# Optimization experiments

Hardware: AMD Instinct MI355X
Metric: run time of the kernel (lower is better)

## Reference

```python
import jax, jax.numpy as jnp
import numpy as np
from jax import lax

B, T, IN, H = 128, 1024, 256, 256


def setup_inputs() -> dict:
    key = jax.random.key(0)
    k1, k2, k3, k4 = jax.random.split(key, 4)
    return {
        "fullx": jax.random.normal(k1, (B, T, IN), dtype=jnp.float32),
        "h": jnp.zeros((B, H), dtype=jnp.float32),
        "c": jnp.zeros((B, H), dtype=jnp.float32),
        "wx": jax.random.normal(k2, (IN, 4 * H), dtype=jnp.float32) / (IN ** 0.5),
        "wh": jax.random.normal(k3, (H, 4 * H), dtype=jnp.float32) / (H ** 0.5),
        "b": jax.random.uniform(k4, (1, 4 * H), dtype=jnp.float32),
    }


def reference(fullx, h, c, wx, wh, b):
    hnum = h.shape[1]

    def step(carry, x_t):
        h, c = carry
        t = x_t @ wx + h @ wh + b  # [B, 4H]
        gate = jax.nn.sigmoid(t[:, : 3 * hnum])
        f = gate[:, :hnum]
        i = gate[:, hnum : 2 * hnum]
        o = gate[:, 2 * hnum : 3 * hnum]
        g = jnp.tanh(t[:, 3 * hnum : 4 * hnum])
        c_new = c * f + g * i
        h_new = jnp.tanh(c_new) * o
        return (h_new, c_new), h_new

    xs = jnp.swapaxes(fullx, 0, 1)  # [T, B, IN]
    (h_f, c_f), hs = lax.scan(step, (h, c), xs)
    fullh = jnp.swapaxes(hs, 0, 1)  # [B, T, H]
    return (fullh, h_f, c_f)
```

## Files before the change

kernel.cpp:

```cpp
#include <hip/hip_runtime.h>
#include <hip/hip_fp16.h>
#include <stdint.h>

#define Tdim 1024
#define INdim 256
#define Hdim 256
#define COLS 1024
#define NSLICE 8
#define NGRP 8
#define GB 16
#define UPB 32
#define CPB 128
#define NTHREADS 512
#define FLAG_STRIDE ((Tdim + 1) * NSLICE)
#define FLAG_BYTES (NGRP * FLAG_STRIDE * 4)
#define HBUF_OFF 266240

typedef _Float16 half8 __attribute__((ext_vector_type(8)));
typedef float f32x4 __attribute__((ext_vector_type(4)));

__device__ __forceinline__ uint16_t f2h(float f) {
    __half h = __float2half(f);
    return *reinterpret_cast<uint16_t*>(&h);
}
__device__ __forceinline__ uint32_t pk2(float lo, float hi) {
    return (uint32_t)f2h(lo) | ((uint32_t)f2h(hi) << 16);
}
__device__ __forceinline__ float sigm(float v) {
    return __builtin_amdgcn_rcpf(1.f + __expf(-v));
}
__device__ __forceinline__ float tanhfast(float v) {
    float e = __expf(2.f * v);
    return 1.f - 2.f * __builtin_amdgcn_rcpf(e + 1.f);
}
__device__ __forceinline__ size_t hb_idx(int par, int grp, int m, int u) {
    return ((((size_t)par * NGRP + grp) * GB + m) << 8) | (size_t)u;
}

__global__ __launch_bounds__(NTHREADS, 1) void lstm_main(
    const float* __restrict__ x, const float* __restrict__ h0,
    const float* __restrict__ c0, const float* __restrict__ wx,
    const float* __restrict__ wh, const float* __restrict__ bias,
    float* __restrict__ out, uint32_t* flags, uint16_t* hbuf)
{
    const int tid   = threadIdx.x;
    const int grp   = blockIdx.x & 7;
    const int slice = blockIdx.x >> 3;
    const int lane  = tid & 63;
    const int wave  = tid >> 6;
    const int cw    = lane & 15;
    const int lhi   = lane >> 4;
    const int cl    = wave * 16 + cw;
    const int g     = cl & 3;
    const int ul    = cl >> 2;
    const int u     = slice * UPB + ul;
    const int gcol  = g * Hdim + u;

    __shared__ __align__(16) uint16_t Wl[CPB * 512];
    __shared__ __align__(16) uint16_t X[2][GB][32][8];
    __shared__ __align__(16) uint16_t Hs[GB][32][8];
    __shared__ __align__(16) uint16_t Hp16[GB][UPB];
    __shared__ __align__(16) float    Hpf[GB][UPB];

    for (int idx = tid; idx < CPB * 512; idx += NTHREADS) {
        int k  = idx >> 7;
        int ci = idx & 127;
        int uu = ci & 31, gg = ci >> 5;
        int cg = gg * Hdim + slice * UPB + uu;
        int c  = (uu << 2) | gg;
        float w = (k < INdim) ? wx[(size_t)k * COLS + cg]
                              : wh[(size_t)(k - INdim) * COLS + cg];
        int e = c * 512 + ((((k >> 3) ^ (c & 7)) << 3) | (k & 7));
        Wl[e] = f2h(w);
    }
    const int m_s   = tid >> 5;
    const int ko_s  = tid & 31;
    const int slt_s = ko_s ^ (m_s & 7);
    {
        const float4* xs = reinterpret_cast<const float4*>(
            &x[((size_t)(grp * GB + m_s) * Tdim + 0) * INdim + ko_s * 8]);
        float4 a = xs[0], b = xs[1];
        uint4 pkv = {pk2(a.x, a.y), pk2(a.z, a.w), pk2(b.x, b.y), pk2(b.z, b.w)};
        *reinterpret_cast<uint4*>(&X[0][m_s][slt_s][0]) = pkv;
    }
    float4 xp0, xp1;
    {
        const float4* xs = reinterpret_cast<const float4*>(
            &x[((size_t)(grp * GB + m_s) * Tdim + 1) * INdim + ko_s * 8]);
        xp0 = xs[0]; xp1 = xs[1];
    }
    if (tid < 64) {
        int m = tid >> 2, uo = tid & 3;
        int u0 = slice * UPB + uo * 8;
        const float4* hs = reinterpret_cast<const float4*>(
            &h0[(size_t)(grp * GB + m) * Hdim + u0]);
        float4 a = hs[0], b = hs[1];
        unsigned long long p0 =
            (unsigned long long)pk2(a.x, a.y) | ((unsigned long long)pk2(a.z, a.w) << 32);
        unsigned long long p1 =
            (unsigned long long)pk2(b.x, b.y) | ((unsigned long long)pk2(b.z, b.w) << 32);
        unsigned long long* hp =
            reinterpret_cast<unsigned long long*>(&hbuf[hb_idx(0, grp, m, u0)]);
        __hip_atomic_store(&hp[0], p0, __ATOMIC_RELAXED, __HIP_MEMORY_SCOPE_AGENT);
        __hip_atomic_store(&hp[1], p1, __ATOMIC_RELAXED, __HIP_MEMORY_SCOPE_AGENT);
    }
    float c_reg[4];
    #pragma unroll
    for (int r = 0; r < 4; ++r)
        c_reg[r] = c0[(size_t)(grp * GB + lhi * 4 + r) * Hdim + u];
    const float bv = bias[gcol];
    __syncthreads();
    uint32_t* fl = flags + grp * FLAG_STRIDE;
    if (tid == 0)
        __hip_atomic_store(&fl[slice], 1u, __ATOMIC_RELAXED, __HIP_MEMORY_SCOPE_AGENT);

    const uint32_t swz = (uint32_t)(cl & 7);
    const uint16_t* wrow = &Wl[cl * 512];
    half8 Wf[16];
    #pragma unroll
    for (int i = 0; i < 16; ++i)
        Wf[i] = *reinterpret_cast<const half8*>(&wrow[(((uint32_t)(i * 4 + lhi)) ^ swz) << 3]);

    const int swz_a = cw & 7;
    float hv[4] = {0.f, 0.f, 0.f, 0.f};

    for (int t = 0; t < Tdim; ++t) {
        const int par = t & 1, pn = par ^ 1;

        {
            uint4 pkv = {pk2(xp0.x, xp0.y), pk2(xp0.z, xp0.w),
                         pk2(xp1.x, xp1.y), pk2(xp1.z, xp1.w)};
            *reinterpret_cast<uint4*>(&X[pn][m_s][slt_s][0]) = pkv;
        }
        {
            int tn = (t + 2 < Tdim) ? t + 2 : Tdim - 1;
            const float4* xs = reinterpret_cast<const float4*>(
                &x[((size_t)(grp * GB + m_s) * Tdim + tn) * INdim + ko_s * 8]);
            xp0 = xs[0]; xp1 = xs[1];
        }

        f32x4 acc0 = {0.f, 0.f, 0.f, 0.f}, acc1 = {0.f, 0.f, 0.f, 0.f};
        #pragma unroll
        for (int s = 0; s < 8; s += 2) {
            int ko0 = s * 4 + lhi, ko1 = ko0 + 4;
            half8 a0 = *reinterpret_cast<const half8*>(&X[par][cw][ko0 ^ swz_a][0]);
            acc0 = __builtin_amdgcn_mfma_f32_16x16x32_f16(a0, Wf[s], acc0, 0, 0, 0);
            half8 a1 = *reinterpret_cast<const half8*>(&X[par][cw][ko1 ^ swz_a][0]);
            acc1 = __builtin_amdgcn_mfma_f32_16x16x32_f16(a1, Wf[s + 1], acc1, 0, 0, 0);
        }

        if (tid < NSLICE) {
            while (__hip_atomic_load(&fl[t * NSLICE + tid], __ATOMIC_RELAXED,
                                     __HIP_MEMORY_SCOPE_AGENT) == 0) {}
        }
        __syncthreads();

        {
            const unsigned long long* hp = reinterpret_cast<const unsigned long long*>(
                &hbuf[hb_idx(par, grp, m_s, ko_s * 8)]);
            unsigned long long h0v = __hip_atomic_load(&hp[0], __ATOMIC_RELAXED,
                                                       __HIP_MEMORY_SCOPE_AGENT);
            unsigned long long h1v = __hip_atomic_load(&hp[1], __ATOMIC_RELAXED,
                                                       __HIP_MEMORY_SCOPE_AGENT);
            uint4 hw = {(uint32_t)h0v, (uint32_t)(h0v >> 32),
                        (uint32_t)h1v, (uint32_t)(h1v >> 32)};
            *reinterpret_cast<uint4*>(&Hs[m_s][slt_s][0]) = hw;
        }
        __syncthreads();

        #pragma unroll
        for (int s = 0; s < 8; s += 2) {
            int ko0 = s * 4 + lhi, ko1 = ko0 + 4;
            half8 a0 = *reinterpret_cast<const half8*>(&Hs[cw][ko0 ^ swz_a][0]);
            acc0 = __builtin_amdgcn_mfma_f32_16x16x32_f16(a0, Wf[8 + s], acc0, 0, 0, 0);
            half8 a1 = *reinterpret_cast<const half8*>(&Hs[cw][ko1 ^ swz_a][0]);
            acc1 = __builtin_amdgcn_mfma_f32_16x16x32_f16(a1, Wf[9 + s], acc1, 0, 0, 0);
        }

        #pragma unroll
        for (int r = 0; r < 4; ++r) {
            float tval = acc0[r] + acc1[r] + bv;
            float act = (g == 3) ? tanhfast(tval) : sigm(tval);
            float x1  = __shfl_xor(act, 1);
            float e0  = (g & 1) ? x1 : act;
            float o1  = (g & 1) ? act : x1;
            float e0s = __shfl_xor(e0, 2);
            float o1s = __shfl_xor(o1, 2);
            float f_ = (g < 2) ? e0  : e0s;
            float i_ = (g < 2) ? o1  : o1s;
            float o_ = (g < 2) ? e0s : e0;
            float g_ = (g < 2) ? o1s : o1;
            c_reg[r] = fmaf(c_reg[r], f_, g_ * i_);
            hv[r] = tanhfast(c_reg[r]) * o_;
        }

        if (g == 0) {
            #pragma unroll
            for (int r = 0; r < 4; ++r) {
                int m = lhi * 4 + r;
                Hp16[m][ul] = f2h(hv[r]);
                Hpf[m][ul]  = hv[r];
            }
        }
        __syncthreads();

        if (tid < 128) {
            int m = tid >> 3, q = tid & 7;
            unsigned long long v =
                *reinterpret_cast<const unsigned long long*>(&Hp16[m][q * 4]);
            __hip_atomic_store(reinterpret_cast<unsigned long long*>(
                                   &hbuf[hb_idx(pn, grp, m, slice * UPB + q * 4)]),
                               v, __ATOMIC_RELAXED, __HIP_MEMORY_SCOPE_AGENT);
        }
        __syncthreads();
        if (tid == 0)
            __hip_atomic_store(&fl[(t + 1) * NSLICE + slice], 1u,
                               __ATOMIC_RELAXED, __HIP_MEMORY_SCOPE_AGENT);

        if (tid >= 128 && tid < 256) {
            int j = tid - 128;
            int m = j >> 3, q = j & 7;
            float4 v = *reinterpret_cast<const float4*>(&Hpf[m][q * 4]);
            *reinterpret_cast<float4*>(
                &out[((size_t)(grp * GB + m) * Tdim + t) * Hdim + slice * UPB + q * 4]) = v;
        }
    }

    if (g == 0) {
        const size_t fsz = (size_t)(NGRP * GB) * Tdim * Hdim;
        #pragma unroll
        for (int r = 0; r < 4; ++r) {
            int m = lhi * 4 + r;
            out[fsz + (size_t)(grp * GB + m) * Hdim + u] = hv[r];
            out[fsz + (size_t)(NGRP * GB) * Hdim + (size_t)(grp * GB + m) * Hdim + u] = c_reg[r];
        }
    }
}

extern "C" void kernel_launch(void* const* d_in, const int* in_sizes, int n_in,
                              void* d_out, int out_size, void* d_ws, size_t ws_size,
                              hipStream_t stream) {
    const float* x    = (const float*)d_in[0];
    const float* h0   = (const float*)d_in[1];
    const float* c0   = (const float*)d_in[2];
    const float* wx   = (const float*)d_in[3];
    const float* wh   = (const float*)d_in[4];
    const float* bias = (const float*)d_in[5];
    float* out = (float*)d_out;
    uint32_t* flags = (uint32_t*)d_ws;
    uint16_t* hbuf  = (uint16_t*)((char*)d_ws + HBUF_OFF);

    hipMemsetAsync(flags, 0, FLAG_BYTES, stream);

    void* args[] = {(void*)&x, (void*)&h0, (void*)&c0, (void*)&wx, (void*)&wh,
                    (void*)&bias, (void*)&out, (void*)&flags, (void*)&hbuf};
    hipLaunchCooperativeKernel((const void*)lstm_main, dim3(NSLICE * NGRP),
                               dim3(NTHREADS), args, 0, stream);
}
```

Before: 2.308 ms.

## Replace per-step flag barrier with tagged h exchange words polled directly

Drops the separate per-step flag array. Each hidden-state fp16 value is now packed with a 16-bit timestep tag into a 32-bit word, and consumers spin on their own h words until every tag matches. This removes the flag spin plus extra __syncthreads, the LDS staging of Hp16/Hpf, and the two-phase store-then-flag publish. Producers write global h and output directly from registers after a shuffle, and the Hs staging buffer reuses the weight LDS region. The cost is doubled exchange traffic, since each value carries a tag, plus more polling loads per thread.

Result: slower. 2.985 ms (+29.3%).

```diff
diff --git a/kernel.cpp b/kernel.cpp
--- a/kernel.cpp
+++ b/kernel.cpp
@@ -12,12 +12,12 @@
 #define UPB 32
 #define CPB 128
 #define NTHREADS 512
-#define FLAG_STRIDE ((Tdim + 1) * NSLICE)
-#define FLAG_BYTES (NGRP * FLAG_STRIDE * 4)
-#define HBUF_OFF 266240
+#define HBUF2_QW (2 * NGRP * GB * 128)
+#define HBUF2_BYTES (HBUF2_QW * 8)
 
 typedef _Float16 half8 __attribute__((ext_vector_type(8)));
 typedef float f32x4 __attribute__((ext_vector_type(4)));
+typedef unsigned long long ull;
 
 __device__ __forceinline__ uint16_t f2h(float f) {
     __half h = __float2half(f);
@@ -33,15 +33,18 @@
     float e = __expf(2.f * v);
     return 1.f - 2.f * __builtin_amdgcn_rcpf(e + 1.f);
 }
-__device__ __forceinline__ size_t hb_idx(int par, int grp, int m, int u) {
-    return ((((size_t)par * NGRP + grp) * GB + m) << 8) | (size_t)u;
+__device__ __forceinline__ size_t gr_idx(int par, int grp, int m, int s16) {
+    return ((((size_t)par * NGRP + grp) * GB + m) << 7) | (size_t)s16;
+}
+__device__ __forceinline__ ull ld_gr(const ull* p) {
+    return __hip_atomic_load(p, __ATOMIC_RELAXED, __HIP_MEMORY_SCOPE_AGENT);
 }
 
 __global__ __launch_bounds__(NTHREADS, 1) void lstm_main(
     const float* __restrict__ x, const float* __restrict__ h0,
     const float* __restrict__ c0, const float* __restrict__ wx,
     const float* __restrict__ wh, const float* __restrict__ bias,
-    float* __restrict__ out, uint32_t* flags, uint16_t* hbuf)
+    float* __restrict__ out, ull* hbuf2)
 {
     const int tid   = threadIdx.x;
     const int grp   = blockIdx.x & 7;
@@ -56,11 +59,11 @@
     const int u     = slice * UPB + ul;
     const int gcol  = g * Hdim + u;
 
-    __shared__ __align__(16) uint16_t Wl[CPB * 512];
+    __shared__ __align__(16) char smem[CPB * 512 * 2];
+    uint16_t* Wl = reinterpret_cast<uint16_t*>(smem);
+    typedef uint16_t HsT[GB][32][8];
+    HsT* Hs2 = reinterpret_cast<HsT*>(smem);
     __shared__ __align__(16) uint16_t X[2][GB][32][8];
-    __shared__ __align__(16) uint16_t Hs[GB][32][8];
-    __shared__ __align__(16) uint16_t Hp16[GB][UPB];
-    __shared__ __align__(16) float    Hpf[GB][UPB];
 
     for (int idx = tid; idx < CPB * 512; idx += NTHREADS) {
         int k  = idx >> 7;
@@ -89,20 +92,15 @@
             &x[((size_t)(grp * GB + m_s) * Tdim + 1) * INdim + ko_s * 8]);
         xp0 = xs[0]; xp1 = xs[1];
     }
-    if (tid < 64) {
-        int m = tid >> 2, uo = tid & 3;
-        int u0 = slice * UPB + uo * 8;
-        const float4* hs = reinterpret_cast<const float4*>(
-            &h0[(size_t)(grp * GB + m) * Hdim + u0]);
-        float4 a = hs[0], b = hs[1];
-        unsigned long long p0 =
-            (unsigned long long)pk2(a.x, a.y) | ((unsigned long long)pk2(a.z, a.w) << 32);
-        unsigned long long p1 =
-            (unsigned long long)pk2(b.x, b.y) | ((unsigned long long)pk2(b.z, b.w) << 32);
-        unsigned long long* hp =
-            reinterpret_cast<unsigned long long*>(&hbuf[hb_idx(0, grp, m, u0)]);
-        __hip_atomic_store(&hp[0], p0, __ATOMIC_RELAXED, __HIP_MEMORY_SCOPE_AGENT);
-        __hip_atomic_store(&hp[1], p1, __ATOMIC_RELAXED, __HIP_MEMORY_SCOPE_AGENT);
+    if (tid < 256) {
+        int m = tid >> 4, j = tid & 15;
+        int u0 = slice * UPB + 2 * j;
+        float a = h0[(size_t)(grp * GB + m) * Hdim + u0];
+        float b = h0[(size_t)(grp * GB + m) * Hdim + u0 + 1];
+        ull v = (ull)(((uint32_t)f2h(a) << 16) | 1u)
+              | ((ull)(((uint32_t)f2h(b) << 16) | 1u) << 32);
+        __hip_atomic_store(&hbuf2[gr_idx(0, grp, m, slice * 16 + j)], v,
+                           __ATOMIC_RELAXED, __HIP_MEMORY_SCOPE_AGENT);
     }
     float c_reg[4];
     #pragma unroll
@@ -110,9 +108,6 @@
         c_reg[r] = c0[(size_t)(grp * GB + lhi * 4 + r) * Hdim + u];
     const float bv = bias[gcol];
     __syncthreads();
-    uint32_t* fl = flags + grp * FLAG_STRIDE;
-    if (tid == 0)
-        __hip_atomic_store(&fl[slice], 1u, __ATOMIC_RELAXED, __HIP_MEMORY_SCOPE_AGENT);
 
     const uint32_t swz = (uint32_t)(cl & 7);
     const uint16_t* wrow = &Wl[cl * 512];
@@ -120,8 +115,11 @@
     #pragma unroll
     for (int i = 0; i < 16; ++i)
         Wf[i] = *reinterpret_cast<const half8*>(&wrow[(((uint32_t)(i * 4 + lhi)) ^ swz) << 3]);
+    __syncthreads();
 
     const int swz_a = cw & 7;
+    const bool pub = (g == 0) && ((ul & 1) == 0);
+    const int s16_pub = slice * 16 + (ul >> 1);
     float hv[4] = {0.f, 0.f, 0.f, 0.f};
 
     for (int t = 0; t < Tdim; ++t) {
@@ -138,6 +136,10 @@
                 &x[((size_t)(grp * GB + m_s) * Tdim + tn) * INdim + ko_s * 8]);
             xp0 = xs[0]; xp1 = xs[1];
         }
+
+        const uint32_t tt = (uint32_t)(t + 1);
+        const ull* gp = hbuf2 + gr_idx(par, grp, m_s, ko_s * 4);
+        ull q0 = ld_gr(gp), q1 = ld_gr(gp + 1), q2 = ld_gr(gp + 2), q3 = ld_gr(gp + 3);
 
         f32x4 acc0 = {0.f, 0.f, 0.f, 0.f}, acc1 = {0.f, 0.f, 0.f, 0.f};
         #pragma unroll
@@ -149,31 +151,27 @@
             acc1 = __builtin_amdgcn_mfma_f32_16x16x32_f16(a1, Wf[s + 1], acc1, 0, 0, 0);
         }
 
-        if (tid < NSLICE) {
-            while (__hip_atomic_load(&fl[t * NSLICE + tid], __ATOMIC_RELAXED,
-                                     __HIP_MEMORY_SCOPE_AGENT) == 0) {}
-        }
-        __syncthreads();
-
+        for (;;) {
+            ull d = ((q0 ^ tt) | ((q0 >> 32) ^ tt) | (q1 ^ tt) | ((q1 >> 32) ^ tt)
+                   | (q2 ^ tt) | ((q2 >> 32) ^ tt) | (q3 ^ tt) | ((q3 >> 32) ^ tt));
+            if (((uint32_t)d & 0xFFFFu) == 0) break;
+            q0 = ld_gr(gp); q1 = ld_gr(gp + 1); q2 = ld_gr(gp + 2); q3 = ld_gr(gp + 3);
+        }
         {
-            const unsigned long long* hp = reinterpret_cast<const unsigned long long*>(
-                &hbuf[hb_idx(par, grp, m_s, ko_s * 8)]);
-            unsigned long long h0v = __hip_atomic_load(&hp[0], __ATOMIC_RELAXED,
-                                                       __HIP_MEMORY_SCOPE_AGENT);
-            unsigned long long h1v = __hip_atomic_load(&hp[1], __ATOMIC_RELAXED,
-                                                       __HIP_MEMORY_SCOPE_AGENT);
-            uint4 hw = {(uint32_t)h0v, (uint32_t)(h0v >> 32),
-                        (uint32_t)h1v, (uint32_t)(h1v >> 32)};
-            *reinterpret_cast<uint4*>(&Hs[m_s][slt_s][0]) = hw;
+            uint4 hw = {(uint32_t)((q0 >> 16) & 0xFFFF) | ((uint32_t)(q0 >> 48) << 16),
+                        (uint32_t)((q1 >> 16) & 0xFFFF) | ((uint32_t)(q1 >> 48) << 16),
+                        (uint32_t)((q2 >> 16) & 0xFFFF) | ((uint32_t)(q2 >> 48) << 16),
+                        (uint32_t)((q3 >> 16) & 0xFFFF) | ((uint32_t)(q3 >> 48) << 16)};
+            *reinterpret_cast<uint4*>(&Hs2[par][m_s][slt_s][0]) = hw;
         }
         __syncthreads();
 
         #pragma unroll
         for (int s = 0; s < 8; s += 2) {
             int ko0 = s * 4 + lhi, ko1 = ko0 + 4;
-            half8 a0 = *reinterpret_cast<const half8*>(&Hs[cw][ko0 ^ swz_a][0]);
+            half8 a0 = *reinterpret_cast<const half8*>(&Hs2[par][cw][ko0 ^ swz_a][0]);
             acc0 = __builtin_amdgcn_mfma_f32_16x16x32_f16(a0, Wf[8 + s], acc0, 0, 0, 0);
-            half8 a1 = *reinterpret_cast<const half8*>(&Hs[cw][ko1 ^ swz_a][0]);
+            half8 a1 = *reinterpret_cast<const half8*>(&Hs2[par][cw][ko1 ^ swz_a][0]);
             acc1 = __builtin_amdgcn_mfma_f32_16x16x32_f16(a1, Wf[9 + s], acc1, 0, 0, 0);
         }
 
@@ -194,35 +192,22 @@
             hv[r] = tanhfast(c_reg[r]) * o_;
         }
 
-        if (g == 0) {
+        float hp[4];
+        #pragma unroll
+        for (int r = 0; r < 4; ++r) hp[r] = __shfl_xor(hv[r], 4);
+        if (pub) {
+            const uint32_t tg = (uint32_t)(t + 2);
             #pragma unroll
             for (int r = 0; r < 4; ++r) {
                 int m = lhi * 4 + r;
-                Hp16[m][ul] = f2h(hv[r]);
-                Hpf[m][ul]  = hv[r];
+                ull v = (ull)(((uint32_t)f2h(hv[r]) << 16) | tg)
+                      | ((ull)(((uint32_t)f2h(hp[r]) << 16) | tg) << 32);
+                __hip_atomic_store(&hbuf2[gr_idx(pn, grp, m, s16_pub)], v,
+                                   __ATOMIC_RELAXED, __HIP_MEMORY_SCOPE_AGENT);
+                float2 o2 = {hv[r], hp[r]};
+                *reinterpret_cast<float2*>(
+                    &out[((size_t)(grp * GB + m) * Tdim + t) * Hdim + u]) = o2;
             }
-        }
-        __syncthreads();
-
-        if (tid < 128) {
-            int m = tid >> 3, q = tid & 7;
-            unsigned long long v =
-                *reinterpret_cast<const unsigned long long*>(&Hp16[m][q * 4]);
-            __hip_atomic_store(reinterpret_cast<unsigned long long*>(
-                                   &hbuf[hb_idx(pn, grp, m, slice * UPB + q * 4)]),
-                               v, __ATOMIC_RELAXED, __HIP_MEMORY_SCOPE_AGENT);
-        }
-        __syncthreads();
-        if (tid == 0)
-            __hip_atomic_store(&fl[(t + 1) * NSLICE + slice], 1u,
-                               __ATOMIC_RELAXED, __HIP_MEMORY_SCOPE_AGENT);
-
-        if (tid >= 128 && tid < 256) {
-            int j = tid - 128;
-            int m = j >> 3, q = j & 7;
-            float4 v = *reinterpret_cast<const float4*>(&Hpf[m][q * 4]);
-            *reinterpret_cast<float4*>(
-                &out[((size_t)(grp * GB + m) * Tdim + t) * Hdim + slice * UPB + q * 4]) = v;
         }
     }
 
@@ -247,13 +232,12 @@
     const float* wh   = (const float*)d_in[4];
     const float* bias = (const float*)d_in[5];
     float* out = (float*)d_out;
-    uint32_t* flags = (uint32_t*)d_ws;
-    uint16_t* hbuf  = (uint16_t*)((char*)d_ws + HBUF_OFF);
-
-    hipMemsetAsync(flags, 0, FLAG_BYTES, stream);
+    ull* hbuf2 = (ull*)d_ws;
+
+    hipMemsetAsync(hbuf2, 0, HBUF2_BYTES, stream);
 
     void* args[] = {(void*)&x, (void*)&h0, (void*)&c0, (void*)&wx, (void*)&wh,
-                    (void*)&bias, (void*)&out, (void*)&flags, (void*)&hbuf};
+                    (void*)&bias, (void*)&out, (void*)&hbuf2};
     hipLaunchCooperativeKernel((const void*)lstm_main, dim3(NSLICE * NGRP),
                                dim3(NTHREADS), args, 0, stream);
 }
```

## Hoist input projection into a parallel GEMM and split recurrence into block pairs

Applied to the files above, without the earlier changes.

Adds a separate xw_gemm kernel that precomputes x·Wx + b for all timesteps into a half-precision workspace buffer. The recurrent kernel is then restructured to 16 blocks, with two blocks per batch group each owning 128 hidden units. Each block exchanges only half of h with its partner through flags, instead of an 8-way all-slice exchange, which shortens the per-step sync chain. The new path needs 256 MB of workspace and otherwise falls back to the old kernel. It also adds fp16 rounding of the precomputed gate inputs and a heavy HBM write plus read of that buffer.

New measurement: 2.995 ms. +29.7%, slower.

```diff
diff --git a/kernel.cpp b/kernel.cpp
--- a/kernel.cpp
+++ b/kernel.cpp
@@ -1,6 +1,278 @@
 #include <hip/hip_runtime.h>
 #include <hip/hip_fp16.h>
 #include <stdint.h>
+
+typedef _Float16 half8 __attribute__((ext_vector_type(8)));
+typedef float f32x4 __attribute__((ext_vector_type(4)));
+typedef unsigned long long ull;
+
+__device__ __forceinline__ uint16_t f2h(float f) {
+    __half h = __float2half(f);
+    return *reinterpret_cast<uint16_t*>(&h);
+}
+__device__ __forceinline__ float h2f(uint16_t b) {
+    return (float)__builtin_bit_cast(_Float16, b);
+}
+__device__ __forceinline__ uint32_t pk2(float lo, float hi) {
+    return (uint32_t)f2h(lo) | ((uint32_t)f2h(hi) << 16);
+}
+__device__ __forceinline__ float sigm(float v) {
+    return __builtin_amdgcn_rcpf(1.f + __expf(-v));
+}
+__device__ __forceinline__ float tanhfast(float v) {
+    float e = __expf(2.f * v);
+    return 1.f - 2.f * __builtin_amdgcn_rcpf(e + 1.f);
+}
+
+#define FL_BYTES 65600
+#define HB_OFF   65664ull
+#define XG_OFF   262144ull
+#define WS_NEEDED (XG_OFF + 268435456ull)
+
+__device__ __forceinline__ size_t HB(int par, int grp, int s, int m, int q) {
+    return (((size_t)((par * 8 + grp) * 2 + s) * 16 + m) * 32 + q);
+}
+__device__ __forceinline__ size_t XGi(int grp, int t, int s, int m, int u) {
+    return ((((size_t)(grp * 1024 + t) * 2 + s) * 16 + m) * 128 + u);
+}
+
+__global__ __launch_bounds__(512, 1) void xw_gemm(
+    const float* __restrict__ x, const float* __restrict__ wx,
+    const float* __restrict__ bias, ull* __restrict__ xg)
+{
+    const int tid = threadIdx.x;
+    const int tc = blockIdx.x >> 4;
+    const int grp = (blockIdx.x >> 1) & 7;
+    const int slice = blockIdx.x & 1;
+    const int lane = tid & 63, wave = tid >> 6;
+    const int cw = lane & 15, lhi = lane >> 4;
+    const int u = wave * 16 + cw;
+
+    __shared__ __align__(16) uint16_t Wxl[512 * 136];
+    __shared__ __align__(16) uint16_t Xl[2][16][33][8];
+
+    half8 Wxf[4][8];
+    #pragma unroll
+    for (int p = 0; p < 2; ++p) {
+        for (int idx = tid; idx < 512 * 128; idx += 512) {
+            int k_l = idx >> 9, c_l = idx & 511;
+            int gg = c_l >> 7, uu = c_l & 127;
+            int col = gg * 256 + slice * 128 + uu;
+            Wxl[c_l * 136 + k_l] = f2h(wx[(size_t)(p * 128 + k_l) * 1024 + col]);
+        }
+        __syncthreads();
+        #pragma unroll
+        for (int g = 0; g < 4; ++g)
+            #pragma unroll
+            for (int jj = 0; jj < 4; ++jj)
+                Wxf[g][p * 4 + jj] = *reinterpret_cast<const half8*>(
+                    &Wxl[(g * 128 + u) * 136 + jj * 32 + lhi * 8]);
+        __syncthreads();
+    }
+    float bv[4];
+    #pragma unroll
+    for (int g = 0; g < 4; ++g) bv[g] = bias[g * 256 + slice * 128 + u];
+
+    const int t0 = tc * 64;
+    const int m_s = tid >> 5, q_s = tid & 31;
+    const float* xrow = &x[((size_t)(grp * 16 + m_s) * 1024) * 256 + q_s * 8];
+    {
+        const float4* xs = reinterpret_cast<const float4*>(xrow + (size_t)t0 * 256);
+        float4 a = xs[0], b = xs[1];
+        uint4 pkv = {pk2(a.x, a.y), pk2(a.z, a.w), pk2(b.x, b.y), pk2(b.z, b.w)};
+        *reinterpret_cast<uint4*>(&Xl[0][m_s][q_s][0]) = pkv;
+    }
+    float4 xa, xb;
+    {
+        const float4* xs = reinterpret_cast<const float4*>(xrow + (size_t)(t0 + 1) * 256);
+        xa = xs[0]; xb = xs[1];
+    }
+    __syncthreads();
+
+    for (int tt = 0; tt < 64; ++tt) {
+        const int t = t0 + tt, buf = tt & 1, bn = buf ^ 1;
+        if (tt < 63) {
+            uint4 pkv = {pk2(xa.x, xa.y), pk2(xa.z, xa.w), pk2(xb.x, xb.y), pk2(xb.z, xb.w)};
+            *reinterpret_cast<uint4*>(&Xl[bn][m_s][q_s][0]) = pkv;
+        }
+        if (tt < 62) {
+            const float4* xs = reinterpret_cast<const float4*>(xrow + (size_t)(t + 2) * 256);
+            xa = xs[0]; xb = xs[1];
+        }
+        f32x4 a0 = {0,0,0,0}, a1 = {0,0,0,0}, a2 = {0,0,0,0}, a3 = {0,0,0,0};
+        #pragma unroll
+        for (int ks = 0; ks < 8; ++ks) {
+            half8 av = *reinterpret_cast<const half8*>(&Xl[buf][cw][ks * 4 + lhi][0]);
+            a0 = __builtin_amdgcn_mfma_f32_16x16x32_f16(av, Wxf[0][ks], a0, 0, 0, 0);
+            a1 = __builtin_amdgcn_mfma_f32_16x16x32_f16(av, Wxf[1][ks], a1, 0, 0, 0);
+            a2 = __builtin_amdgcn_mfma_f32_16x16x32_f16(av, Wxf[2][ks], a2, 0, 0, 0);
+            a3 = __builtin_amdgcn_mfma_f32_16x16x32_f16(av, Wxf[3][ks], a3, 0, 0, 0);
+        }
+        #pragma unroll
+        for (int r = 0; r < 4; ++r) {
+            ull v = (ull)f2h(a0[r] + bv[0])
+                  | ((ull)f2h(a1[r] + bv[1]) << 16)
+                  | ((ull)f2h(a2[r] + bv[2]) << 32)
+                  | ((ull)f2h(a3[r] + bv[3]) << 48);
+            xg[XGi(grp, t, slice, lhi * 4 + r, u)] = v;
+        }
+        __syncthreads();
+    }
+}
+
+__global__ __launch_bounds__(512, 1) void lstm_pair(
+    const float* __restrict__ h0, const float* __restrict__ c0,
+    const float* __restrict__ wh, float* __restrict__ out,
+    uint32_t* flags, ull* hbuf, const ull* __restrict__ xg)
+{
+    const int tid = threadIdx.x;
+    const int grp = blockIdx.x >> 1;
+    const int slice = blockIdx.x & 1;
+    const int lane = tid & 63, wave = tid >> 6;
+    const int cw = lane & 15, lhi = lane >> 4;
+    const int u = wave * 16 + cw;
+    const int gu = slice * 128 + u;
+
+    __shared__ __align__(16) uint16_t Whl[512 * 136];
+    __shared__ __align__(16) uint16_t Hs2[2][16][33][8];
+
+    half8 Wf[4][8];
+    #pragma unroll
+    for (int p = 0; p < 2; ++p) {
+        for (int idx = tid; idx < 512 * 128; idx += 512) {
+            int k_l = idx >> 9, c_l = idx & 511;
+            int gg = c_l >> 7, uu = c_l & 127;
+            int col = gg * 256 + slice * 128 + uu;
+            Whl[c_l * 136 + k_l] = f2h(wh[(size_t)(p * 128 + k_l) * 1024 + col]);
+        }
+        __syncthreads();
+        if (slice == p) {
+            #pragma unroll
+            for (int g = 0; g < 4; ++g)
+                #pragma unroll
+                for (int jj = 0; jj < 4; ++jj)
+                    Wf[g][jj] = *reinterpret_cast<const half8*>(
+                        &Whl[(g * 128 + u) * 136 + jj * 32 + lhi * 8]);
+        } else {
+            #pragma unroll
+            for (int g = 0; g < 4; ++g)
+                #pragma unroll
+                for (int jj = 0; jj < 4; ++jj)
+                    Wf[g][4 + jj] = *reinterpret_cast<const half8*>(
+                        &Whl[(g * 128 + u) * 136 + jj * 32 + lhi * 8]);
+        }
+        __syncthreads();
+    }
+
+    const int m_s = tid >> 5, q_s = tid & 31;
+    {
+        const float4* hp = reinterpret_cast<const float4*>(
+            &h0[(size_t)(grp * 16 + m_s) * 256 + q_s * 8]);
+        float4 a = hp[0], b = hp[1];
+        uint4 pkv = {pk2(a.x, a.y), pk2(a.z, a.w), pk2(b.x, b.y), pk2(b.z, b.w)};
+        *reinterpret_cast<uint4*>(&Hs2[0][m_s][q_s][0]) = pkv;
+    }
+    float c_reg[4];
+    #pragma unroll
+    for (int r = 0; r < 4; ++r)
+        c_reg[r] = c0[(size_t)(grp * 16 + lhi * 4 + r) * 256 + gu];
+
+    const size_t xg_base = (size_t)grp * 4194304 + (size_t)slice * 2048 + (size_t)u;
+    ull xq0 = xg[xg_base + (lhi * 4 + 0) * 128];
+    ull xq1 = xg[xg_base + (lhi * 4 + 1) * 128];
+    ull xq2 = xg[xg_base + (lhi * 4 + 2) * 128];
+    ull xq3 = xg[xg_base + (lhi * 4 + 3) * 128];
+    __syncthreads();
+
+    uint32_t* flA = flags + (grp * 2 + slice) * 1025;
+    uint32_t* flB = flags + (grp * 2 + (1 - slice)) * 1025;
+    const int koA = slice * 16;
+    const int koB = 16 - koA;
+    const int ko_w = gu >> 3, e_w = gu & 7;
+    float* outrow0 = &out[((size_t)(grp * 16) * 1024) * 256 + gu];
+    float hv[4] = {0.f, 0.f, 0.f, 0.f};
+
+    for (int t = 0; t < 1024; ++t) {
+        const int par = t & 1, pn = par ^ 1;
+
+        f32x4 a0 = {0,0,0,0}, a1 = {0,0,0,0}, a2 = {0,0,0,0}, a3 = {0,0,0,0};
+        #pragma unroll
+        for (int jj = 0; jj < 4; ++jj) {
+            half8 av = *reinterpret_cast<const half8*>(&Hs2[par][cw][koA + jj * 4 + lhi][0]);
+            a0 = __builtin_amdgcn_mfma_f32_16x16x32_f16(av, Wf[0][jj], a0, 0, 0, 0);
+            a1 = __builtin_amdgcn_mfma_f32_16x16x32_f16(av, Wf[1][jj], a1, 0, 0, 0);
+            a2 = __builtin_amdgcn_mfma_f32_16x16x32_f16(av, Wf[2][jj], a2, 0, 0, 0);
+            a3 = __builtin_amdgcn_mfma_f32_16x16x32_f16(av, Wf[3][jj], a3, 0, 0, 0);
+        }
+        asm volatile("s_waitcnt vmcnt(0)" ::: "memory");
+        __syncthreads();
+        if (t > 0 && tid == 0)
+            __hip_atomic_store(&flA[t], 1u, __ATOMIC_RELAXED, __HIP_MEMORY_SCOPE_AGENT);
+
+        int tn = (t + 1 < 1024) ? t + 1 : t;
+        const size_t xb = xg_base + (size_t)tn * 4096;
+        ull nx0 = xg[xb + (lhi * 4 + 0) * 128];
+        ull nx1 = xg[xb + (lhi * 4 + 1) * 128];
+        ull nx2 = xg[xb + (lhi * 4 + 2) * 128];
+        ull nx3 = xg[xb + (lhi * 4 + 3) * 128];
+
+        if (t > 0) {
+            while (__hip_atomic_load(&flB[t], __ATOMIC_RELAXED,
+                                     __HIP_MEMORY_SCOPE_AGENT) == 0) {}
+            ull pg = __hip_atomic_load(&hbuf[HB(par, grp, 1 - slice, m_s, q_s)],
+                                       __ATOMIC_RELAXED, __HIP_MEMORY_SCOPE_AGENT);
+            *reinterpret_cast<ull*>(&Hs2[par][m_s][koB + (q_s >> 1)][(q_s & 1) * 4]) = pg;
+        }
+        __syncthreads();
+
+        #pragma unroll
+        for (int jj = 0; jj < 4; ++jj) {
+            half8 av = *reinterpret_cast<const half8*>(&Hs2[par][cw][koB + jj * 4 + lhi][0]);
+            a0 = __builtin_amdgcn_mfma_f32_16x16x32_f16(av, Wf[0][4 + jj], a0, 0, 0, 0);
+            a1 = __builtin_amdgcn_mfma_f32_16x16x32_f16(av, Wf[1][4 + jj], a1, 0, 0, 0);
+            a2 = __builtin_amdgcn_mfma_f32_16x16x32_f16(av, Wf[2][4 + jj], a2, 0, 0, 0);
+            a3 = __builtin_amdgcn_mfma_f32_16x16x32_f16(av, Wf[3][4 + jj], a3, 0, 0, 0);
+        }
+
+        #define GATES(r, xq)                                                        \
+        {                                                                           \
+            float tf = a0[r] + h2f((uint16_t)(xq));                                 \
+            float ti = a1[r] + h2f((uint16_t)((xq) >> 16));                         \
+            float to = a2[r] + h2f((uint16_t)((xq) >> 32));                         \
+            float tg = a3[r] + h2f((uint16_t)((xq) >> 48));                         \
+            float fg = sigm(tf), ig = sigm(ti), og = sigm(to), gv = tanhfast(tg);   \
+            c_reg[r] = fmaf(c_reg[r], fg, gv * ig);                                 \
+            hv[r] = tanhfast(c_reg[r]) * og;                                        \
+        }
+        GATES(0, xq0) GATES(1, xq1) GATES(2, xq2) GATES(3, xq3)
+        #undef GATES
+
+        #pragma unroll
+        for (int r = 0; r < 4; ++r)
+            outrow0[((size_t)(lhi * 4 + r) * 1024 + t) * 256] = hv[r];
+
+        #pragma unroll
+        for (int r = 0; r < 4; ++r)
+            Hs2[pn][lhi * 4 + r][ko_w][e_w] = f2h(hv[r]);
+        __syncthreads();
+
+        {
+            ull v = *reinterpret_cast<const ull*>(
+                &Hs2[pn][m_s][koA + (q_s >> 1)][(q_s & 1) * 4]);
+            __hip_atomic_store(&hbuf[HB(pn, grp, slice, m_s, q_s)], v,
+                               __ATOMIC_RELAXED, __HIP_MEMORY_SCOPE_AGENT);
+        }
+        xq0 = nx0; xq1 = nx1; xq2 = nx2; xq3 = nx3;
+    }
+
+    const size_t fsz = (size_t)128 * 1024 * 256;
+    #pragma unroll
+    for (int r = 0; r < 4; ++r) {
+        int b = grp * 16 + lhi * 4 + r;
+        out[fsz + (size_t)b * 256 + gu] = hv[r];
+        out[fsz + (size_t)128 * 256 + (size_t)b * 256 + gu] = c_reg[r];
+    }
+}
 
 #define Tdim 1024
 #define INdim 256
@@ -12,32 +284,15 @@
 #define UPB 32
 #define CPB 128
 #define NTHREADS 512
-#define FLAG_STRIDE ((Tdim + 1) * NSLICE)
-#define FLAG_BYTES (NGRP * FLAG_STRIDE * 4)
-#define HBUF_OFF 266240
-
-typedef _Float16 half8 __attribute__((ext_vector_type(8)));
-typedef float f32x4 __attribute__((ext_vector_type(4)));
-
-__device__ __forceinline__ uint16_t f2h(float f) {
-    __half h = __float2half(f);
-    return *reinterpret_cast<uint16_t*>(&h);
-}
-__device__ __forceinline__ uint32_t pk2(float lo, float hi) {
-    return (uint32_t)f2h(lo) | ((uint32_t)f2h(hi) << 16);
-}
-__device__ __forceinline__ float sigm(float v) {
-    return __builtin_amdgcn_rcpf(1.f + __expf(-v));
-}
-__device__ __forceinline__ float tanhfast(float v) {
-    float e = __expf(2.f * v);
-    return 1.f - 2.f * __builtin_amdgcn_rcpf(e + 1.f);
-}
-__device__ __forceinline__ size_t hb_idx(int par, int grp, int m, int u) {
+#define FB_FLAG_STRIDE ((Tdim + 1) * NSLICE)
+#define FB_FLAG_BYTES (NGRP * FB_FLAG_STRIDE * 4)
+#define FB_HBUF_OFF 266240
+
+__device__ __forceinline__ size_t hbF_idx(int par, int grp, int m, int u) {
     return ((((size_t)par * NGRP + grp) * GB + m) << 8) | (size_t)u;
 }
 
-__global__ __launch_bounds__(NTHREADS, 1) void lstm_main(
+__global__ __launch_bounds__(NTHREADS, 1) void lstm_fallback(
     const float* __restrict__ x, const float* __restrict__ h0,
     const float* __restrict__ c0, const float* __restrict__ wx,
     const float* __restrict__ wh, const float* __restrict__ bias,
@@ -95,12 +350,9 @@
         const float4* hs = reinterpret_cast<const float4*>(
             &h0[(size_t)(grp * GB + m) * Hdim + u0]);
         float4 a = hs[0], b = hs[1];
-        unsigned long long p0 =
-            (unsigned long long)pk2(a.x, a.y) | ((unsigned long long)pk2(a.z, a.w) << 32);
-        unsigned long long p1 =
-            (unsigned long long)pk2(b.x, b.y) | ((unsigned long long)pk2(b.z, b.w) << 32);
-        unsigned long long* hp =
-            reinterpret_cast<unsigned long long*>(&hbuf[hb_idx(0, grp, m, u0)]);
+        ull p0 = (ull)pk2(a.x, a.y) | ((ull)pk2(a.z, a.w) << 32);
+        ull p1 = (ull)pk2(b.x, b.y) | ((ull)pk2(b.z, b.w) << 32);
+        ull* hp = reinterpret_cast<ull*>(&hbuf[hbF_idx(0, grp, m, u0)]);
         __hip_atomic_store(&hp[0], p0, __ATOMIC_RELAXED, __HIP_MEMORY_SCOPE_AGENT);
         __hip_atomic_store(&hp[1], p1, __ATOMIC_RELAXED, __HIP_MEMORY_SCOPE_AGENT);
     }
@@ -110,7 +362,7 @@
         c_reg[r] = c0[(size_t)(grp * GB + lhi * 4 + r) * Hdim + u];
     const float bv = bias[gcol];
     __syncthreads();
-    uint32_t* fl = flags + grp * FLAG_STRIDE;
+    uint32_t* fl = flags + grp * FB_FLAG_STRIDE;
     if (tid == 0)
         __hip_atomic_store(&fl[slice], 1u, __ATOMIC_RELAXED, __HIP_MEMORY_SCOPE_AGENT);
 
@@ -126,7 +378,6 @@
 
     for (int t = 0; t < Tdim; ++t) {
         const int par = t & 1, pn = par ^ 1;
-
         {
             uint4 pkv = {pk2(xp0.x, xp0.y), pk2(xp0.z, xp0.w),
                          pk2(xp1.x, xp1.y), pk2(xp1.z, xp1.w)};
@@ -138,45 +389,38 @@
                 &x[((size_t)(grp * GB + m_s) * Tdim + tn) * INdim + ko_s * 8]);
             xp0 = xs[0]; xp1 = xs[1];
         }
-
         f32x4 acc0 = {0.f, 0.f, 0.f, 0.f}, acc1 = {0.f, 0.f, 0.f, 0.f};
         #pragma unroll
         for (int s = 0; s < 8; s += 2) {
             int ko0 = s * 4 + lhi, ko1 = ko0 + 4;
-            half8 a0 = *reinterpret_cast<const half8*>(&X[par][cw][ko0 ^ swz_a][0]);
-            acc0 = __builtin_amdgcn_mfma_f32_16x16x32_f16(a0, Wf[s], acc0, 0, 0, 0);
-            half8 a1 = *reinterpret_cast<const half8*>(&X[par][cw][ko1 ^ swz_a][0]);
-            acc1 = __builtin_amdgcn_mfma_f32_16x16x32_f16(a1, Wf[s + 1], acc1, 0, 0, 0);
-        }
-
+            half8 av0 = *reinterpret_cast<const half8*>(&X[par][cw][ko0 ^ swz_a][0]);
+            acc0 = __builtin_amdgcn_mfma_f32_16x16x32_f16(av0, Wf[s], acc0, 0, 0, 0);
+            half8 av1 = *reinterpret_cast<const half8*>(&X[par][cw][ko1 ^ swz_a][0]);
+            acc1 = __builtin_amdgcn_mfma_f32_16x16x32_f16(av1, Wf[s + 1], acc1, 0, 0, 0);
+        }
         if (tid < NSLICE) {
             while (__hip_atomic_load(&fl[t * NSLICE + tid], __ATOMIC_RELAXED,
                                      __HIP_MEMORY_SCOPE_AGENT) == 0) {}
         }
         __syncthreads();
-
         {
-            const unsigned long long* hp = reinterpret_cast<const unsigned long long*>(
-                &hbuf[hb_idx(par, grp, m_s, ko_s * 8)]);
-            unsigned long long h0v = __hip_atomic_load(&hp[0], __ATOMIC_RELAXED,
-                                                       __HIP_MEMORY_SCOPE_AGENT);
-            unsigned long long h1v = __hip_atomic_load(&hp[1], __ATOMIC_RELAXED,
-                                                       __HIP_MEMORY_SCOPE_AGENT);
+            const ull* hp = reinterpret_cast<const ull*>(
+                &hbuf[hbF_idx(par, grp, m_s, ko_s * 8)]);
+            ull h0v = __hip_atomic_load(&hp[0], __ATOMIC_RELAXED, __HIP_MEMORY_SCOPE_AGENT);
+            ull h1v = __hip_atomic_load(&hp[1], __ATOMIC_RELAXED, __HIP_MEMORY_SCOPE_AGENT);
             uint4 hw = {(uint32_t)h0v, (uint32_t)(h0v >> 32),
                         (uint32_t)h1v, (uint32_t)(h1v >> 32)};
             *reinterpret_cast<uint4*>(&Hs[m_s][slt_s][0]) = hw;
         }
         __syncthreads();
-
         #pragma unroll
         for (int s = 0; s < 8; s += 2) {
             int ko0 = s * 4 + lhi, ko1 = ko0 + 4;
-            half8 a0 = *reinterpret_cast<const half8*>(&Hs[cw][ko0 ^ swz_a][0]);
-            acc0 = __builtin_amdgcn_mfma_f32_16x16x32_f16(a0, Wf[8 + s], acc0, 0, 0, 0);
-            half8 a1 = *reinterpret_cast<const half8*>(&Hs[cw][ko1 ^ swz_a][0]);
-            acc1 = __builtin_amdgcn_mfma_f32_16x16x32_f16(a1, Wf[9 + s], acc1, 0, 0, 0);
-        }
-
+            half8 av0 = *reinterpret_cast<const half8*>(&Hs[cw][ko0 ^ swz_a][0]);
+            acc0 = __builtin_amdgcn_mfma_f32_16x16x32_f16(av0, Wf[8 + s], acc0, 0, 0, 0);
+            half8 av1 = *reinterpret_cast<const half8*>(&Hs[cw][ko1 ^ swz_a][0]);
+            acc1 = __builtin_amdgcn_mfma_f32_16x16x32_f16(av1, Wf[9 + s], acc1, 0, 0, 0);
+        }
         #pragma unroll
         for (int r = 0; r < 4; ++r) {
             float tval = acc0[r] + acc1[r] + bv;
@@ -193,7 +437,6 @@
             c_reg[r] = fmaf(c_reg[r], f_, g_ * i_);
             hv[r] = tanhfast(c_reg[r]) * o_;
         }
-
         if (g == 0) {
             #pragma unroll
             for (int r = 0; r < 4; ++r) {
@@ -203,20 +446,18 @@
             }
         }
         __syncthreads();
-
         if (tid < 128) {
             int m = tid >> 3, q = tid & 7;
-            unsigned long long v =
-                *reinterpret_cast<const unsigned long long*>(&Hp16[m][q * 4]);
-            __hip_atomic_store(reinterpret_cast<unsigned long long*>(
-                                   &hbuf[hb_idx(pn, grp, m, slice * UPB + q * 4)]),
+            ull v = *reinterpret_cast<const ull*>(&Hp16[m][q * 4]);
+            __hip_atomic_store(reinterpret_cast<ull*>(
+                                   &hbuf[hbF_idx(pn, grp, m, slice * UPB + q * 4)]),
                                v, __ATOMIC_RELAXED, __HIP_MEMORY_SCOPE_AGENT);
         }
+        asm volatile("s_waitcnt vmcnt(0)" ::: "memory");
         __syncthreads();
         if (tid == 0)
             __hip_atomic_store(&fl[(t + 1) * NSLICE + slice], 1u,
                                __ATOMIC_RELAXED, __HIP_MEMORY_SCOPE_AGENT);
-
         if (tid >= 128 && tid < 256) {
             int j = tid - 128;
             int m = j >> 3, q = j & 7;
@@ -225,7 +466,6 @@
                 &out[((size_t)(grp * GB + m) * Tdim + t) * Hdim + slice * UPB + q * 4]) = v;
         }
     }
-
     if (g == 0) {
         const size_t fsz = (size_t)(NGRP * GB) * Tdim * Hdim;
         #pragma unroll
@@ -247,13 +487,24 @@
     const float* wh   = (const float*)d_in[4];
     const float* bias = (const float*)d_in[5];
     float* out = (float*)d_out;
-    uint32_t* flags = (uint32_t*)d_ws;
-    uint16_t* hbuf  = (uint16_t*)((char*)d_ws + HBUF_OFF);
-
-    hipMemsetAsync(flags, 0, FLAG_BYTES, stream);
-
-    void* args[] = {(void*)&x, (void*)&h0, (void*)&c0, (void*)&wx, (void*)&wh,
-                    (void*)&bias, (void*)&out, (void*)&flags, (void*)&hbuf};
-    hipLaunchCooperativeKernel((const void*)lstm_main, dim3(NSLICE * NGRP),
-                               dim3(NTHREADS), args, 0, stream);
-}
+
+    if (ws_size >= WS_NEEDED) {
+        uint32_t* flags = (uint32_t*)d_ws;
+        ull* hbuf = (ull*)((char*)d_ws + HB_OFF);
+        ull* xgp  = (ull*)((char*)d_ws + XG_OFF);
+        hipMemsetAsync(d_ws, 0, FL_BYTES, stream);
+        xw_gemm<<<256, 512, 0, stream>>>(x, wx, bias, xgp);
+        void* args[] = {(void*)&h0, (void*)&c0, (void*)&wh, (void*)&out,
+                        (void*)&flags, (void*)&hbuf, (void*)&xgp};
+        hipLaunchCooperativeKernel((const void*)lstm_pair, dim3(16), dim3(512),
+                                   args, 0, stream);
+    } else {
+        uint32_t* flags = (uint32_t*)d_ws;
+        uint16_t* hbuf  = (uint16_t*)((char*)d_ws + FB_HBUF_OFF);
+        hipMemsetAsync(flags, 0, FB_FLAG_BYTES, stream);
+        void* args[] = {(void*)&x, (void*)&h0, (void*)&c0, (void*)&wx, (void*)&wh,
+                        (void*)&bias, (void*)&out, (void*)&flags, (void*)&hbuf};
+        hipLaunchCooperativeKernel((const void*)lstm_fallback, dim3(NSLICE * NGRP),
+                                   dim3(NTHREADS), args, 0, stream);
+    }
+}
```
